# Optimization experiments

Hardware: AMD Instinct MI355X
Metric: run time of the kernel (lower is better)

Reference implementation:

```python
import jax, jax.numpy as jnp
import numpy as np

TEMPERATURE = 0.07


def _l2_normalize(x, axis=-1, eps=1e-12):
    # matches torch F.normalize: x / max(||x||, eps)
    n = jnp.sqrt(jnp.sum(x * x, axis=axis, keepdims=True))
    return x / jnp.maximum(n, eps)


def setup_inputs() -> dict:
    key = jax.random.key(0)
    k1, k2, k3 = jax.random.split(key, 3)
    B, C, H, W = 1024, 256, 24, 24
    img_features = jax.random.normal(k1, (B, C, H, W), dtype=jnp.float32)
    text_embeds = jax.random.normal(k2, (B, C), dtype=jnp.float32)
    labels = jax.random.randint(k3, (B,), 0, 16, dtype=jnp.int64)
    return {"img_features": img_features, "text_embeds": text_embeds, "labels": labels}


def reference(img_features, text_embeds, labels):
    # adaptive_avg_pool2d to 1x1 == global mean over H,W -> [B, C]
    img_pooled = img_features.mean(axis=(2, 3))
    img_pooled = _l2_normalize(img_pooled, axis=1)
    text_n = _l2_normalize(text_embeds, axis=1)
    logits = (img_pooled @ text_n.T) / TEMPERATURE  # [B, B]
    # vectorized label equality replaces the O(N^2) python loop
    targets = (labels[:, None] == labels[None, :]).astype(logits.dtype)
    # BCE with logits, mean reduction: logaddexp(0, x) - x*z
    loss = jnp.mean(jnp.logaddexp(0.0, logits) - logits * targets)
    return loss
```

## Files before the change

### kernel.cpp

```cpp
#include <hip/hip_runtime.h>
#include <math.h>

static constexpr int B_N  = 1024;
static constexpr int C_N  = 256;
static constexpr int HW_N = 576;
static constexpr float TEMP_INV = 1.0f / 0.07f;

typedef __attribute__((ext_vector_type(8))) short bf16x8;
typedef __attribute__((ext_vector_type(4))) float f32x4;
typedef __attribute__((ext_vector_type(4))) float f4v;

static __device__ __forceinline__ unsigned short f2bf(float f) {
    unsigned u = __float_as_uint(f);
    return (unsigned short)((u + 0x7FFFu + ((u >> 16) & 1u)) >> 16);
}

__global__ __launch_bounds__(256) void pool_kernel(const float* __restrict__ img,
                                                   const float* __restrict__ text,
                                                   float* __restrict__ pooled,
                                                   unsigned short* __restrict__ Bb,
                                                   float* __restrict__ loss_acc,
                                                   unsigned int* __restrict__ ticket) {
    const int t    = threadIdx.x;
    const int w    = t >> 6;
    const int lane = t & 63;

    if (blockIdx.x < 32) {
        if (blockIdx.x == 0 && t == 0) { *loss_acc = 0.0f; *ticket = 0u; }
        const int r0 = blockIdx.x * 32 + w * 8;
        #pragma unroll
        for (int rr = 0; rr < 8; ++rr) {
            const int r = r0 + rr;
            const f4v v = ((const f4v*)(text + (size_t)r * C_N))[lane];
            float ss = v.x * v.x + v.y * v.y + v.z * v.z + v.w * v.w;
            #pragma unroll
            for (int off = 32; off > 0; off >>= 1) ss += __shfl_xor(ss, off, 64);
            const float inv = 1.0f / fmaxf(sqrtf(ss), 1e-12f);
            ushort4 o;
            o.x = f2bf(v.x * inv); o.y = f2bf(v.y * inv);
            o.z = f2bf(v.z * inv); o.w = f2bf(v.w * inv);
            ((ushort4*)(Bb + (size_t)r * C_N))[lane] = o;
        }
        return;
    }

    const int g = blockIdx.x - 32;
    const size_t ch4 = (size_t)g * 16 + (size_t)w * 4;
    const f4v* src = (const f4v*)img + ch4 * 144;

    f4v vv[9];
    #pragma unroll
    for (int j = 0; j < 9; ++j)
        vv[j] = __builtin_nontemporal_load(&src[j * 64 + lane]);

    float a0 = 0.f, a1 = 0.f, a2 = 0.f, a3 = 0.f;
    #pragma unroll
    for (int j = 0; j < 9; ++j) {
        const int idx = j * 64 + lane;
        const float s = (vv[j].x + vv[j].y) + (vv[j].z + vv[j].w);
        a0 += (idx < 144)               ? s : 0.0f;
        a1 += (idx >= 144 && idx < 288) ? s : 0.0f;
        a2 += (idx >= 288 && idx < 432) ? s : 0.0f;
        a3 += (idx >= 432)              ? s : 0.0f;
    }

    #pragma unroll
    for (int off = 32; off > 0; off >>= 1) {
        a0 += __shfl_xor(a0, off, 64);
        a1 += __shfl_xor(a1, off, 64);
        a2 += __shfl_xor(a2, off, 64);
        a3 += __shfl_xor(a3, off, 64);
    }
    if (lane == 0) {
        const float sc = 1.0f / (float)HW_N;
        f4v o; o.x = a0 * sc; o.y = a1 * sc; o.z = a2 * sc; o.w = a3 * sc;
        ((f4v*)pooled)[ch4 >> 2] = o;
    }
}

__global__ __launch_bounds__(256) void prep_kernel(const float* __restrict__ pooled,
                                                   unsigned short* __restrict__ Ab) {
    const int w    = threadIdx.x >> 6;
    const int lane = threadIdx.x & 63;
    const int r = blockIdx.x * 4 + w;
    const float4 v = ((const float4*)(pooled + (size_t)r * C_N))[lane];
    float ss = v.x * v.x + v.y * v.y + v.z * v.z + v.w * v.w;
    #pragma unroll
    for (int off = 32; off > 0; off >>= 1) ss += __shfl_xor(ss, off, 64);
    const float inv = 1.0f / fmaxf(sqrtf(ss), 1e-12f);
    ushort4 o;
    o.x = f2bf(v.x * inv); o.y = f2bf(v.y * inv);
    o.z = f2bf(v.z * inv); o.w = f2bf(v.w * inv);
    ((ushort4*)(Ab + (size_t)r * C_N))[lane] = o;
}

__global__ __launch_bounds__(256) void gemm_loss_kernel(const unsigned short* __restrict__ Ab,
                                                        const unsigned short* __restrict__ Bb,
                                                        const int* __restrict__ labels,
                                                        float* __restrict__ loss_acc,
                                                        unsigned int* __restrict__ ticket,
                                                        float* __restrict__ out) {
    __shared__ unsigned short Abuf[64 * 256];
    __shared__ unsigned short Bbuf[64 * 256];

    const int t = threadIdx.x;
    const int rowBase = (blockIdx.x & 15) << 6;
    const int colBase = (blockIdx.x >> 4) << 6;

    #pragma unroll
    for (int i = 0; i < 8; ++i) {
        const int c   = t + (i << 8);
        const int row = c >> 5;
        const int kc  = c & 31;
        const unsigned off = (unsigned)((row << 9) + (kc << 4)) ^ (unsigned)((row & 7) << 4);
        uint4 va = ((const uint4*)(Ab + (size_t)(rowBase + row) * C_N))[kc];
        *(uint4*)((char*)Abuf + off) = va;
        uint4 vb = ((const uint4*)(Bb + (size_t)(colBase + row) * C_N))[kc];
        *(uint4*)((char*)Bbuf + off) = vb;
    }
    __syncthreads();

    const int w    = t >> 6;
    const int lane = t & 63;
    const int m16  = lane & 15;
    const int kg   = lane >> 4;

    f32x4 acc[4] = {{0.f, 0.f, 0.f, 0.f}, {0.f, 0.f, 0.f, 0.f},
                    {0.f, 0.f, 0.f, 0.f}, {0.f, 0.f, 0.f, 0.f}};

    #pragma unroll
    for (int s = 0; s < 8; ++s) {
        const int kc   = (s << 2) + kg;
        const int arow = (w << 4) + m16;
        const bf16x8 a = *(const bf16x8*)((char*)Abuf +
                            (((unsigned)((arow << 9) + (kc << 4))) ^ (unsigned)((arow & 7) << 4)));
        #pragma unroll
        for (int ct = 0; ct < 4; ++ct) {
            const int brow = (ct << 4) + m16;
            const bf16x8 b = *(const bf16x8*)((char*)Bbuf +
                                (((unsigned)((brow << 9) + (kc << 4))) ^ (unsigned)((brow & 7) << 4)));
            acc[ct] = __builtin_amdgcn_mfma_f32_16x16x32_bf16(a, b, acc[ct], 0, 0, 0);
        }
    }

    float lsum = 0.0f;
    const int gi0 = rowBase + (w << 4) + (kg << 2);
    int labi[4];
    #pragma unroll
    for (int r = 0; r < 4; ++r) labi[r] = labels[gi0 + r];
    #pragma unroll
    for (int ct = 0; ct < 4; ++ct) {
        const int gj = colBase + (ct << 4) + m16;
        const int labj = labels[gj];
        #pragma unroll
        for (int r = 0; r < 4; ++r) {
            const float x = acc[ct][r] * TEMP_INV;
            const float z = (labi[r] == labj) ? 1.0f : 0.0f;
            const float sp = fmaxf(x, 0.0f) + __logf(1.0f + __expf(-fabsf(x)));
            lsum += sp - x * z;
        }
    }

    #pragma unroll
    for (int off = 32; off > 0; off >>= 1) lsum += __shfl_xor(lsum, off, 64);
    __syncthreads();
    float* red = (float*)Abuf;
    if ((t & 63) == 0) red[w] = lsum;
    __syncthreads();
    if (t == 0) {
        const float bsum = red[0] + red[1] + red[2] + red[3];
        atomicAdd(loss_acc, bsum);
        __threadfence();
        const unsigned old = atomicAdd(ticket, 1u);
        if (old == 255u) {
            const float total = atomicAdd(loss_acc, 0.0f);
            out[0] = total * (1.0f / ((float)B_N * (float)B_N));
        }
    }
}

extern "C" void kernel_launch(void* const* d_in, const int* in_sizes, int n_in,
                              void* d_out, int out_size, void* d_ws, size_t ws_size,
                              hipStream_t stream) {
    const float* img    = (const float*)d_in[0];
    const float* text   = (const float*)d_in[1];
    const int*   labels = (const int*)d_in[2];
    float* out = (float*)d_out;

    char* ws = (char*)d_ws;
    unsigned short* Ab       = (unsigned short*)ws;
    unsigned short* Bb       = (unsigned short*)(ws + (512 << 10));
    float*          pooled   = (float*)(ws + (1 << 20));
    float*          loss_acc = (float*)(ws + (2 << 20));
    unsigned int*   ticket   = (unsigned int*)(ws + (2 << 20) + 4);

    pool_kernel<<<32 + 16384, 256, 0, stream>>>(img, text, pooled, Bb, loss_acc, ticket);
    prep_kernel<<<256, 256, 0, stream>>>(pooled, Ab);
    gemm_loss_kernel<<<256, 256, 0, stream>>>(Ab, Bb, labels, loss_acc, ticket, out);
}
```

Before: 108.7 us.

## Fuse image-row normalization into GEMM epilogue, drop prep kernel

```diff
diff --git a/kernel.cpp b/kernel.cpp
--- a/kernel.cpp
+++ b/kernel.cpp
@@ -15,9 +15,13 @@
     return (unsigned short)((u + 0x7FFFu + ((u >> 16) & 1u)) >> 16);
 }
 
+static __device__ __forceinline__ float bf2f(unsigned short h) {
+    return __uint_as_float(((unsigned)h) << 16);
+}
+
 __global__ __launch_bounds__(256) void pool_kernel(const float* __restrict__ img,
                                                    const float* __restrict__ text,
-                                                   float* __restrict__ pooled,
+                                                   unsigned short* __restrict__ Ab,
                                                    unsigned short* __restrict__ Bb,
                                                    float* __restrict__ loss_acc,
                                                    unsigned int* __restrict__ ticket) {
@@ -73,25 +77,11 @@
     }
     if (lane == 0) {
         const float sc = 1.0f / (float)HW_N;
-        f4v o; o.x = a0 * sc; o.y = a1 * sc; o.z = a2 * sc; o.w = a3 * sc;
-        ((f4v*)pooled)[ch4 >> 2] = o;
-    }
-}
-
-__global__ __launch_bounds__(256) void prep_kernel(const float* __restrict__ pooled,
-                                                   unsigned short* __restrict__ Ab) {
-    const int w    = threadIdx.x >> 6;
-    const int lane = threadIdx.x & 63;
-    const int r = blockIdx.x * 4 + w;
-    const float4 v = ((const float4*)(pooled + (size_t)r * C_N))[lane];
-    float ss = v.x * v.x + v.y * v.y + v.z * v.z + v.w * v.w;
-    #pragma unroll
-    for (int off = 32; off > 0; off >>= 1) ss += __shfl_xor(ss, off, 64);
-    const float inv = 1.0f / fmaxf(sqrtf(ss), 1e-12f);
-    ushort4 o;
-    o.x = f2bf(v.x * inv); o.y = f2bf(v.y * inv);
-    o.z = f2bf(v.z * inv); o.w = f2bf(v.w * inv);
-    ((ushort4*)(Ab + (size_t)r * C_N))[lane] = o;
+        ushort4 o;
+        o.x = f2bf(a0 * sc); o.y = f2bf(a1 * sc);
+        o.z = f2bf(a2 * sc); o.w = f2bf(a3 * sc);
+        ((ushort4*)Ab)[ch4 >> 2] = o;
+    }
 }
 
 __global__ __launch_bounds__(256) void gemm_loss_kernel(const unsigned short* __restrict__ Ab,
@@ -102,6 +92,7 @@
                                                         float* __restrict__ out) {
     __shared__ unsigned short Abuf[64 * 256];
     __shared__ unsigned short Bbuf[64 * 256];
+    __shared__ float invA[64];
 
     const int t = threadIdx.x;
     const int rowBase = (blockIdx.x & 15) << 6;
@@ -120,6 +111,27 @@
     }
     __syncthreads();
 
+    {
+        const int row = t >> 2;
+        const int q   = t & 3;
+        float ss = 0.0f;
+        #pragma unroll
+        for (int j = 0; j < 8; ++j) {
+            const int kc = (q << 3) + j;
+            const unsigned off = (unsigned)((row << 9) + (kc << 4)) ^ (unsigned)((row & 7) << 4);
+            const bf16x8 v = *(const bf16x8*)((char*)Abuf + off);
+            #pragma unroll
+            for (int e = 0; e < 8; ++e) {
+                const float f = bf2f((unsigned short)v[e]);
+                ss += f * f;
+            }
+        }
+        ss += __shfl_xor(ss, 1, 64);
+        ss += __shfl_xor(ss, 2, 64);
+        if (q == 0) invA[row] = 1.0f / fmaxf(sqrtf(ss), 1e-12f);
+    }
+    __syncthreads();
+
     const int w    = t >> 6;
     const int lane = t & 63;
     const int m16  = lane & 15;
@@ -144,17 +156,20 @@
     }
 
     float lsum = 0.0f;
-    const int gi0 = rowBase + (w << 4) + (kg << 2);
-    int labi[4];
-    #pragma unroll
-    for (int r = 0; r < 4; ++r) labi[r] = labels[gi0 + r];
+    const int lr0 = (w << 4) + (kg << 2);
+    float sA[4]; int labi[4];
+    #pragma unroll
+    for (int r = 0; r < 4; ++r) {
+        sA[r]   = invA[lr0 + r] * TEMP_INV;
+        labi[r] = labels[rowBase + lr0 + r];
+    }
     #pragma unroll
     for (int ct = 0; ct < 4; ++ct) {
         const int gj = colBase + (ct << 4) + m16;
         const int labj = labels[gj];
         #pragma unroll
         for (int r = 0; r < 4; ++r) {
-            const float x = acc[ct][r] * TEMP_INV;
+            const float x = acc[ct][r] * sA[r];
             const float z = (labi[r] == labj) ? 1.0f : 0.0f;
             const float sp = fmaxf(x, 0.0f) + __logf(1.0f + __expf(-fabsf(x)));
             lsum += sp - x * z;
@@ -190,11 +205,9 @@
     char* ws = (char*)d_ws;
     unsigned short* Ab       = (unsigned short*)ws;
     unsigned short* Bb       = (unsigned short*)(ws + (512 << 10));
-    float*          pooled   = (float*)(ws + (1 << 20));
-    float*          loss_acc = (float*)(ws + (2 << 20));
-    unsigned int*   ticket   = (unsigned int*)(ws + (2 << 20) + 4);
-
-    pool_kernel<<<32 + 16384, 256, 0, stream>>>(img, text, pooled, Bb, loss_acc, ticket);
-    prep_kernel<<<256, 256, 0, stream>>>(pooled, Ab);
+    float*          loss_acc = (float*)(ws + (1 << 20));
+    unsigned int*   ticket   = (unsigned int*)(ws + (1 << 20) + 4);
+
+    pool_kernel<<<32 + 16384, 256, 0, stream>>>(img, text, Ab, Bb, loss_acc, ticket);
     gemm_loss_kernel<<<256, 256, 0, stream>>>(Ab, Bb, labels, loss_acc, ticket, out);
 }
```

New measurement: 105.3 us. -3.2%, faster.
